# Kernel optimization log

Measured on AMD Instinct MI355X. Metric: run time of the kernel, lower is better.

Reference implementation:

```python
import jax, jax.numpy as jnp
import numpy as np

B, T, C = 8, 2048, 768
H = 1  # n_heads
EPS = 1e-5


def layer_norm(x, g, b):
    mu = jnp.mean(x, axis=-1, keepdims=True)
    var = jnp.mean(jnp.square(x - mu), axis=-1, keepdims=True)
    return (x - mu) * jax.lax.rsqrt(var + EPS) * g + b


def setup_inputs() -> dict:
    key = jax.random.key(0)
    ks = jax.random.split(key, 12)
    s = 1.0 / np.sqrt(C)
    return {
        "x": jax.random.normal(ks[0], (B, T, C), jnp.float32),
        "Wq": jax.random.normal(ks[1], (C, C), jnp.float32) * s,
        "Wk": jax.random.normal(ks[2], (C, C), jnp.float32) * s,
        "Wv": jax.random.normal(ks[3], (C, C), jnp.float32) * s,
        "Wp": jax.random.normal(ks[4], (C, C), jnp.float32) * s,
        "bp": jnp.zeros((C,), jnp.float32),
        "g1": jnp.ones((C,), jnp.float32),
        "b1": jnp.zeros((C,), jnp.float32),
        "g2": jnp.ones((C,), jnp.float32),
        "b2": jnp.zeros((C,), jnp.float32),
        "W1": jax.random.normal(ks[5], (C, 4 * C), jnp.float32) * s,
        "bm1": jnp.zeros((4 * C,), jnp.float32),
        "W2": jax.random.normal(ks[6], (4 * C, C), jnp.float32) * (1.0 / np.sqrt(4 * C)),
        "bm2": jnp.zeros((C,), jnp.float32),
    }


def attention(xn, Wq, Wk, Wv, Wp, bp):
    # single head (H=1): q,k,v are [B, T, C]
    q = xn @ Wq
    k = xn @ Wk
    v = xn @ Wv
    scale = 1.0 / np.sqrt(C // H)
    scores = jnp.einsum("btc,bsc->bts", q, k) * scale  # [B,T,T]
    causal = jnp.tril(jnp.ones((T, T), dtype=bool))
    scores = jnp.where(causal, scores, -jnp.inf)
    attn = jax.nn.softmax(scores, axis=-1)
    y = jnp.einsum("bts,bsc->btc", attn, v)
    return y @ Wp + bp


def reference(x, Wq, Wk, Wv, Wp, bp, g1, b1, g2, b2, W1, bm1, W2, bm2):
    # pre-LN transformer block; dropout is identity at eval
    x = x + attention(layer_norm(x, g1, b1), Wq, Wk, Wv, Wp, bp)
    h = layer_norm(x, g2, b2)
    h = jax.nn.gelu(h @ W1 + bm1, approximate=False) @ W2 + bm2
    return x + h
```

## Files before the change

### kernel.cpp

```cpp
#include <hip/hip_runtime.h>
#include <hip/hip_bf16.h>


typedef unsigned short u16;
typedef __bf16 bf16x8 __attribute__((ext_vector_type(8)));
typedef float  f32x4  __attribute__((ext_vector_type(4)));
typedef int    i32x4  __attribute__((ext_vector_type(4)));
typedef u16    u16x4  __attribute__((ext_vector_type(4)));

__device__ __forceinline__ u16 f2b(float f) {
    __hip_bfloat16 h = __float2bfloat16(f);
    return *reinterpret_cast<u16*>(&h);
}
__device__ __forceinline__ float b2f(u16 u) {
    unsigned int x = ((unsigned int)u) << 16;
    return __uint_as_float(x);
}

__device__ __forceinline__ void stage16(u16* lds_base_uniform, const u16* g, int lane) {
#if __has_builtin(__builtin_amdgcn_global_load_lds)
    __builtin_amdgcn_global_load_lds(
        (const __attribute__((address_space(1))) void*)g,
        (__attribute__((address_space(3))) void*)lds_base_uniform,
        16, 0, 0);
#else
    *(i32x4*)(lds_base_uniform + lane * 8) = *(const i32x4*)g;
#endif
}

__global__ __launch_bounds__(256) void transpose_cast(const float* __restrict__ in,
                                                      u16* __restrict__ out,
                                                      int R, int Cc) {
    __shared__ float tile[32][33];
    int c0 = blockIdx.x * 32, r0 = blockIdx.y * 32;
    int tx = threadIdx.x, ty = threadIdx.y;
    for (int i = ty; i < 32; i += 8)
        tile[i][tx] = in[(long)(r0 + i) * Cc + c0 + tx];
    __syncthreads();
    for (int i = ty; i < 32; i += 8)
        out[(long)(c0 + i) * R + r0 + tx] = f2b(tile[tx][i]);
}

__global__ __launch_bounds__(256) void ln_kernel(const float* __restrict__ x,
                                                 const float* __restrict__ g,
                                                 const float* __restrict__ b,
                                                 u16* __restrict__ out) {
    const int C = 768;
    long row = blockIdx.x;
    const float* xr = x + row * C;
    int t = threadIdx.x;
    float v0 = xr[t], v1 = xr[t + 256], v2 = xr[t + 512];
    float s = v0 + v1 + v2;
    float sq = v0 * v0 + v1 * v1 + v2 * v2;
#pragma unroll
    for (int o = 32; o; o >>= 1) {
        s += __shfl_xor(s, o);
        sq += __shfl_xor(sq, o);
    }
    __shared__ float ss[4], sq2[4];
    int wv = t >> 6;
    if ((t & 63) == 0) { ss[wv] = s; sq2[wv] = sq; }
    __syncthreads();
    s = ss[0] + ss[1] + ss[2] + ss[3];
    sq = sq2[0] + sq2[1] + sq2[2] + sq2[3];
    float mu = s * (1.0f / 768.0f);
    float var = sq * (1.0f / 768.0f) - mu * mu;
    float rs = rsqrtf(var + 1e-5f);
    u16* orow = out + row * C;
    orow[t]       = f2b((v0 - mu) * rs * g[t]       + b[t]);
    orow[t + 256] = f2b((v1 - mu) * rs * g[t + 256] + b[t + 256]);
    orow[t + 512] = f2b((v2 - mu) * rs * g[t + 512] + b[t + 512]);
}

__global__ __launch_bounds__(256) void softmax_causal(u16* __restrict__ S) {
    const int T = 2048;
    long row = blockIdx.x;
    int t = (int)(row & (T - 1));
    u16* p = S + row * T;
    int tid = threadIdx.x;
    float v[8];
    float mx = -3.0e38f;
#pragma unroll
    for (int j = 0; j < 8; j++) {
        int col = tid + j * 256;
        v[j] = (col <= t) ? b2f(p[col]) : -3.0e38f;
        mx = fmaxf(mx, v[j]);
    }
#pragma unroll
    for (int o = 32; o; o >>= 1) mx = fmaxf(mx, __shfl_xor(mx, o));
    __shared__ float sm[4], ssum[4];
    int wv = tid >> 6;
    if ((tid & 63) == 0) sm[wv] = mx;
    __syncthreads();
    mx = fmaxf(fmaxf(sm[0], sm[1]), fmaxf(sm[2], sm[3]));
    float s = 0.0f;
#pragma unroll
    for (int j = 0; j < 8; j++) {
        int col = tid + j * 256;
        float e = (col <= t) ? expf(v[j] - mx) : 0.0f;
        v[j] = e;
        s += e;
    }
#pragma unroll
    for (int o = 32; o; o >>= 1) s += __shfl_xor(s, o);
    if ((tid & 63) == 0) ssum[wv] = s;
    __syncthreads();
    s = ssum[0] + ssum[1] + ssum[2] + ssum[3];
    float inv = 1.0f / s;
#pragma unroll
    for (int j = 0; j < 8; j++) {
        int col = tid + j * 256;
        p[col] = f2b(v[j] * inv);
    }
}

#define BM 128
#define BN 128
#define BKT 64

template <int EPI, int CAUSAL>
__global__ __launch_bounds__(256) void gemm_bt(const u16* __restrict__ A,
                                               const u16* __restrict__ Bt,
                                               void* __restrict__ Out,
                                               const float* __restrict__ bias,
                                               const float* __restrict__ resid,
                                               int M, int N, int K,
                                               int lda, int ldb, int ldo,
                                               long long sA, long long sB, long long sO,
                                               float scale) {
    int bz = blockIdx.z;
    A += (long)bz * sA;
    Bt += (long)bz * sB;
    long obase = (long)bz * sO;

    int m0 = blockIdx.y * BM, n0 = blockIdx.x * BN;
    if (CAUSAL == 1 && n0 >= m0 + BM) return;
    int kend = (CAUSAL == 2) ? ((K < m0 + BM) ? K : (m0 + BM)) : K;

    __shared__ __align__(16) u16 As[128 * 64];
    __shared__ __align__(16) u16 Bs[128 * 64];

    int tid = threadIdx.x;
    int lane = tid & 63, l16 = lane & 15, quad = lane >> 4;
    int w = tid >> 6;
    int wm = (w >> 1) * 64, wn = (w & 1) * 64;

    f32x4 acc[4][4] = {};

    for (int k0 = 0; k0 < kend; k0 += BKT) {
#pragma unroll
        for (int i = 0; i < 4; i++) {
            int ebase = i * 256 + w * 64;
            int e = ebase + lane;
            int row = e >> 3;
            int gc = (e & 7) ^ (row & 7);
            stage16(As + ebase * 8, A + (long)(m0 + row) * lda + k0 + gc * 8, lane);
            stage16(Bs + ebase * 8, Bt + (long)(n0 + row) * ldb + k0 + gc * 8, lane);
        }
        __syncthreads();
#pragma unroll
        for (int kk = 0; kk < BKT; kk += 32) {
            int cbase = (kk >> 3) + quad;
            int slot = (cbase ^ (l16 & 7)) << 3;
            bf16x8 af[4], bf[4];
#pragma unroll
            for (int mt = 0; mt < 4; mt++)
                af[mt] = *(const bf16x8*)(As + (wm + mt * 16 + l16) * 64 + slot);
#pragma unroll
            for (int nt = 0; nt < 4; nt++)
                bf[nt] = *(const bf16x8*)(Bs + (wn + nt * 16 + l16) * 64 + slot);
#pragma unroll
            for (int mt = 0; mt < 4; mt++)
#pragma unroll
                for (int nt = 0; nt < 4; nt++)
                    acc[mt][nt] = __builtin_amdgcn_mfma_f32_16x16x32_bf16(af[mt], bf[nt], acc[mt][nt], 0, 0, 0);
        }
        __syncthreads();
    }

#pragma unroll
    for (int mt = 0; mt < 4; ++mt)
#pragma unroll
        for (int nt = 0; nt < 4; ++nt) {
            int col = n0 + wn + nt * 16 + l16;
            int rbase = m0 + wm + mt * 16 + quad * 4;
            f32x4 a = acc[mt][nt];
            if (EPI == 0) {
                u16* o = (u16*)Out + obase;
#pragma unroll
                for (int r = 0; r < 4; r++)
                    o[(long)(rbase + r) * ldo + col] = f2b(a[r] * scale);
            } else if (EPI == 1) {
                u16* o = (u16*)Out + obase;
                u16x4 pk;
#pragma unroll
                for (int r = 0; r < 4; r++) pk[r] = f2b(a[r] * scale);
                *(u16x4*)(o + (long)col * ldo + rbase) = pk;
            } else if (EPI == 2) {
                u16* o = (u16*)Out + obase;
                float bv = bias[col];
#pragma unroll
                for (int r = 0; r < 4; r++) {
                    float v = a[r] + bv;
                    float ge = 0.5f * v * (1.0f + erff(v * 0.70710678118f));
                    o[(long)(rbase + r) * ldo + col] = f2b(ge);
                }
            } else {
                float* o = (float*)Out + obase;
                float bv = bias[col];
#pragma unroll
                for (int r = 0; r < 4; r++) {
                    long idx = (long)(rbase + r) * ldo + col;
                    o[idx] = resid[idx] + a[r] + bv;
                }
            }
        }
}

extern "C" void kernel_launch(void* const* d_in, const int* in_sizes, int n_in,
                              void* d_out, int out_size, void* d_ws, size_t ws_size,
                              hipStream_t stream) {
    (void)in_sizes; (void)n_in; (void)out_size; (void)ws_size;
    const float* x   = (const float*)d_in[0];
    const float* Wq  = (const float*)d_in[1];
    const float* Wk  = (const float*)d_in[2];
    const float* Wv  = (const float*)d_in[3];
    const float* Wp  = (const float*)d_in[4];
    const float* bp  = (const float*)d_in[5];
    const float* g1  = (const float*)d_in[6];
    const float* b1  = (const float*)d_in[7];
    const float* g2  = (const float*)d_in[8];
    const float* b2  = (const float*)d_in[9];
    const float* W1  = (const float*)d_in[10];
    const float* bm1 = (const float*)d_in[11];
    const float* W2  = (const float*)d_in[12];
    const float* bm2 = (const float*)d_in[13];
    float* out = (float*)d_out;

    const int Bn = 8, T = 2048, C = 768, F = 3072;
    const int M = Bn * T;

    char* ws = (char*)d_ws;
    u16* xn = (u16*)(ws);
    u16* q  = (u16*)(ws + 25165824);
    u16* kb = (u16*)(ws + 50331648);
    u16* vT = (u16*)(ws + 75497472);
    u16* S  = (u16*)(ws + 100663296);
    u16* y  = (u16*)(ws + 167772160);
    u16* h1 = (u16*)(ws + 25165824);
    u16* wgt = (u16*)(ws + 192937984);
    u16* Wqt = wgt;
    u16* Wkt = Wqt + 589824;
    u16* Wvt = Wkt + 589824;
    u16* Wpt = Wvt + 589824;
    u16* W1t = Wpt + 589824;
    u16* W2t = W1t + (long)C * F;

    dim3 tb(32, 8);
    hipLaunchKernelGGL(transpose_cast, dim3(C / 32, C / 32), tb, 0, stream, Wq, Wqt, C, C);
    hipLaunchKernelGGL(transpose_cast, dim3(C / 32, C / 32), tb, 0, stream, Wk, Wkt, C, C);
    hipLaunchKernelGGL(transpose_cast, dim3(C / 32, C / 32), tb, 0, stream, Wv, Wvt, C, C);
    hipLaunchKernelGGL(transpose_cast, dim3(C / 32, C / 32), tb, 0, stream, Wp, Wpt, C, C);
    hipLaunchKernelGGL(transpose_cast, dim3(F / 32, C / 32), tb, 0, stream, W1, W1t, C, F);
    hipLaunchKernelGGL(transpose_cast, dim3(C / 32, F / 32), tb, 0, stream, W2, W2t, F, C);

    hipLaunchKernelGGL(ln_kernel, dim3(M), dim3(256), 0, stream, x, g1, b1, xn);

    hipLaunchKernelGGL((gemm_bt<0, 0>), dim3(C / BN, M / BM, 1), dim3(256), 0, stream,
                       xn, Wqt, (void*)q, nullptr, nullptr, M, C, C, C, C, C, 0LL, 0LL, 0LL, 1.0f);
    hipLaunchKernelGGL((gemm_bt<0, 0>), dim3(C / BN, M / BM, 1), dim3(256), 0, stream,
                       xn, Wkt, (void*)kb, nullptr, nullptr, M, C, C, C, C, C, 0LL, 0LL, 0LL, 1.0f);
    hipLaunchKernelGGL((gemm_bt<1, 0>), dim3(C / BN, T / BM, Bn), dim3(256), 0, stream,
                       xn, Wvt, (void*)vT, nullptr, nullptr, T, C, C, C, C, T,
                       (long long)T * C, 0LL, (long long)C * T, 1.0f);

    float scl = 1.0f / sqrtf((float)C);
    hipLaunchKernelGGL((gemm_bt<0, 1>), dim3(T / BN, T / BM, Bn), dim3(256), 0, stream,
                       q, kb, (void*)S, nullptr, nullptr, T, T, C, C, C, T,
                       (long long)T * C, (long long)T * C, (long long)T * T, scl);

    hipLaunchKernelGGL(softmax_causal, dim3(M), dim3(256), 0, stream, S);

    hipLaunchKernelGGL((gemm_bt<0, 2>), dim3(C / BN, T / BM, Bn), dim3(256), 0, stream,
                       S, vT, (void*)y, nullptr, nullptr, T, C, T, T, T, C,
                       (long long)T * T, (long long)C * T, (long long)T * C, 1.0f);

    hipLaunchKernelGGL((gemm_bt<3, 0>), dim3(C / BN, M / BM, 1), dim3(256), 0, stream,
                       y, Wpt, (void*)out, bp, x, M, C, C, C, C, C, 0LL, 0LL, 0LL, 1.0f);

    hipLaunchKernelGGL(ln_kernel, dim3(M), dim3(256), 0, stream, out, g2, b2, xn);

    hipLaunchKernelGGL((gemm_bt<2, 0>), dim3(F / BN, M / BM, 1), dim3(256), 0, stream,
                       xn, W1t, (void*)h1, bm1, nullptr, M, F, C, C, C, F, 0LL, 0LL, 0LL, 1.0f);

    hipLaunchKernelGGL((gemm_bt<3, 0>), dim3(C / BN, M / BM, 1), dim3(256), 0, stream,
                       h1, W2t, (void*)out, bm2, out, M, C, F, F, F, C, 0LL, 0LL, 0LL, 1.0f);
}
```

Baseline: 745.4 us.

## Fuse QKV projections, swizzle GEMM tiles across XCDs, trim causal softmax

The three Q/K/V projection GEMMs become one GEMM over the contiguous transposed weights, with an N of 3C. A new epilogue writes Q and K interleaved into one buffer and V transposed into a second one, and the score GEMM reads Q and K from that shared buffer with a stride of 1536. GEMM block indices are remapped so that consecutive tiles are spread across the 8 XCD chunks, aiming for better L2 locality. The causal softmax now stops at the 128-aligned column bound and skips fully masked columns, which the PV GEMM never reads. The remap assumes the tile count is divisible by 8, and the new epilogue hardcodes the shape constants.

```diff
diff --git a/kernel.cpp b/kernel.cpp
--- a/kernel.cpp
+++ b/kernel.cpp
@@ -76,6 +76,7 @@
     const int T = 2048;
     long row = blockIdx.x;
     int t = (int)(row & (T - 1));
+    int ncols = ((t >> 7) + 1) << 7;
     u16* p = S + row * T;
     int tid = threadIdx.x;
     float v[8];
@@ -85,6 +86,7 @@
         int col = tid + j * 256;
         v[j] = (col <= t) ? b2f(p[col]) : -3.0e38f;
         mx = fmaxf(mx, v[j]);
+        if (col >= ncols) break;
     }
 #pragma unroll
     for (int o = 32; o; o >>= 1) mx = fmaxf(mx, __shfl_xor(mx, o));
@@ -97,6 +99,7 @@
 #pragma unroll
     for (int j = 0; j < 8; j++) {
         int col = tid + j * 256;
+        if (col >= ncols) break;
         float e = (col <= t) ? expf(v[j] - mx) : 0.0f;
         v[j] = e;
         s += e;
@@ -110,6 +113,7 @@
 #pragma unroll
     for (int j = 0; j < 8; j++) {
         int col = tid + j * 256;
+        if (col >= ncols) break;
         p[col] = f2b(v[j] * inv);
     }
 }
@@ -122,6 +126,7 @@
 __global__ __launch_bounds__(256) void gemm_bt(const u16* __restrict__ A,
                                                const u16* __restrict__ Bt,
                                                void* __restrict__ Out,
+                                               void* __restrict__ Out2,
                                                const float* __restrict__ bias,
                                                const float* __restrict__ resid,
                                                int M, int N, int K,
@@ -133,7 +138,14 @@
     Bt += (long)bz * sB;
     long obase = (long)bz * sO;
 
-    int m0 = blockIdx.y * BM, n0 = blockIdx.x * BN;
+    int gx = gridDim.x;
+    int nblk = gx * gridDim.y;
+    int lin = blockIdx.y * gx + blockIdx.x;
+    int chunk = nblk >> 3;
+    int tile = (lin & 7) * chunk + (lin >> 3);
+    int m0 = (tile / gx) * BM;
+    int n0 = (tile % gx) * BN;
+
     if (CAUSAL == 1 && n0 >= m0 + BM) return;
     int kend = (CAUSAL == 2) ? ((K < m0 + BM) ? K : (m0 + BM)) : K;
 
@@ -205,13 +217,27 @@
                     float ge = 0.5f * v * (1.0f + erff(v * 0.70710678118f));
                     o[(long)(rbase + r) * ldo + col] = f2b(ge);
                 }
-            } else {
+            } else if (EPI == 3) {
                 float* o = (float*)Out + obase;
                 float bv = bias[col];
 #pragma unroll
                 for (int r = 0; r < 4; r++) {
                     long idx = (long)(rbase + r) * ldo + col;
                     o[idx] = resid[idx] + a[r] + bv;
+                }
+            } else {
+                if (col < 1536) {
+                    u16* o = (u16*)Out;
+#pragma unroll
+                    for (int r = 0; r < 4; r++)
+                        o[(long)(rbase + r) * 1536 + col] = f2b(a[r]);
+                } else {
+                    u16* o = (u16*)Out2;
+                    int b = rbase >> 11, t = rbase & 2047, c = col - 1536;
+                    u16x4 pk;
+#pragma unroll
+                    for (int r = 0; r < 4; r++) pk[r] = f2b(a[r]);
+                    *(u16x4*)(o + ((long)b * 768 + c) * 2048 + t) = pk;
                 }
             }
         }
@@ -242,8 +268,7 @@
 
     char* ws = (char*)d_ws;
     u16* xn = (u16*)(ws);
-    u16* q  = (u16*)(ws + 25165824);
-    u16* kb = (u16*)(ws + 50331648);
+    u16* QK = (u16*)(ws + 25165824);
     u16* vT = (u16*)(ws + 75497472);
     u16* S  = (u16*)(ws + 100663296);
     u16* y  = (u16*)(ws + 167772160);
@@ -266,33 +291,34 @@
 
     hipLaunchKernelGGL(ln_kernel, dim3(M), dim3(256), 0, stream, x, g1, b1, xn);
 
-    hipLaunchKernelGGL((gemm_bt<0, 0>), dim3(C / BN, M / BM, 1), dim3(256), 0, stream,
-                       xn, Wqt, (void*)q, nullptr, nullptr, M, C, C, C, C, C, 0LL, 0LL, 0LL, 1.0f);
-    hipLaunchKernelGGL((gemm_bt<0, 0>), dim3(C / BN, M / BM, 1), dim3(256), 0, stream,
-                       xn, Wkt, (void*)kb, nullptr, nullptr, M, C, C, C, C, C, 0LL, 0LL, 0LL, 1.0f);
-    hipLaunchKernelGGL((gemm_bt<1, 0>), dim3(C / BN, T / BM, Bn), dim3(256), 0, stream,
-                       xn, Wvt, (void*)vT, nullptr, nullptr, T, C, C, C, C, T,
-                       (long long)T * C, 0LL, (long long)C * T, 1.0f);
+    hipLaunchKernelGGL((gemm_bt<4, 0>), dim3((3 * C) / BN, M / BM, 1), dim3(256), 0, stream,
+                       xn, Wqt, (void*)QK, (void*)vT, nullptr, nullptr,
+                       M, 3 * C, C, C, C, 0, 0LL, 0LL, 0LL, 1.0f);
 
     float scl = 1.0f / sqrtf((float)C);
     hipLaunchKernelGGL((gemm_bt<0, 1>), dim3(T / BN, T / BM, Bn), dim3(256), 0, stream,
-                       q, kb, (void*)S, nullptr, nullptr, T, T, C, C, C, T,
-                       (long long)T * C, (long long)T * C, (long long)T * T, scl);
+                       QK, QK + 768, (void*)S, nullptr, nullptr, nullptr,
+                       T, T, C, 1536, 1536, T,
+                       (long long)T * 1536, (long long)T * 1536, (long long)T * T, scl);
 
     hipLaunchKernelGGL(softmax_causal, dim3(M), dim3(256), 0, stream, S);
 
     hipLaunchKernelGGL((gemm_bt<0, 2>), dim3(C / BN, T / BM, Bn), dim3(256), 0, stream,
-                       S, vT, (void*)y, nullptr, nullptr, T, C, T, T, T, C,
+                       S, vT, (void*)y, nullptr, nullptr, nullptr,
+                       T, C, T, T, T, C,
                        (long long)T * T, (long long)C * T, (long long)T * C, 1.0f);
 
     hipLaunchKernelGGL((gemm_bt<3, 0>), dim3(C / BN, M / BM, 1), dim3(256), 0, stream,
-                       y, Wpt, (void*)out, bp, x, M, C, C, C, C, C, 0LL, 0LL, 0LL, 1.0f);
+                       y, Wpt, (void*)out, nullptr, bp, x,
+                       M, C, C, C, C, C, 0LL, 0LL, 0LL, 1.0f);
 
     hipLaunchKernelGGL(ln_kernel, dim3(M), dim3(256), 0, stream, out, g2, b2, xn);
 
     hipLaunchKernelGGL((gemm_bt<2, 0>), dim3(F / BN, M / BM, 1), dim3(256), 0, stream,
-                       xn, W1t, (void*)h1, bm1, nullptr, M, F, C, C, C, F, 0LL, 0LL, 0LL, 1.0f);
+                       xn, W1t, (void*)h1, nullptr, bm1, nullptr,
+                       M, F, C, C, C, F, 0LL, 0LL, 0LL, 1.0f);
 
     hipLaunchKernelGGL((gemm_bt<3, 0>), dim3(C / BN, M / BM, 1), dim3(256), 0, stream,
-                       h1, W2t, (void*)out, bm2, out, M, C, F, F, F, C, 0LL, 0LL, 0LL, 1.0f);
-}
+                       h1, W2t, (void*)out, nullptr, bm2, out,
+                       M, C, F, F, F, C, 0LL, 0LL, 0LL, 1.0f);
+}
```

Result: faster. 695.8 us (-6.7%).
